# Optimization experiments

Measured on AMD Instinct MI355X. Metric: run time of the kernel, lower is better.

Reference implementation:

```python
import jax, jax.numpy as jnp
import numpy as np

D_MODEL = 1024
D_STATE = 16
D_CONV = 4
EXPAND = 2
D_INNER = D_MODEL * EXPAND


def setup_inputs() -> dict:
    key = jax.random.key(0)
    ks = jax.random.split(key, 10)
    B, L = 2, 2048
    x = jax.random.normal(ks[0], (B, L, D_MODEL), jnp.float32)
    W_in = jax.random.normal(ks[1], (2 * D_INNER, D_MODEL), jnp.float32) * (1.0 / np.sqrt(D_MODEL))
    conv_w = jax.random.normal(ks[2], (D_INNER, 1, D_CONV), jnp.float32) * (1.0 / np.sqrt(D_CONV))
    conv_b = jax.random.normal(ks[3], (D_INNER,), jnp.float32) * 0.1
    W_x = jax.random.normal(ks[4], (2 * D_STATE + 1, D_INNER), jnp.float32) * (1.0 / np.sqrt(D_INNER))
    A_log = jnp.log(jnp.abs(jax.random.normal(ks[5], (D_INNER, D_STATE), jnp.float32)) + 1e-4)
    D_param = jnp.ones((D_INNER,), jnp.float32)
    W_dt = jax.random.normal(ks[6], (D_INNER, 1), jnp.float32)
    b_dt = jax.random.normal(ks[7], (D_INNER,), jnp.float32) * 0.1
    W_out = jax.random.normal(ks[8], (D_MODEL, D_INNER), jnp.float32) * (1.0 / np.sqrt(D_INNER))
    return {"x": x, "W_in": W_in, "conv_w": conv_w, "conv_b": conv_b, "W_x": W_x,
            "A_log": A_log, "D_param": D_param, "W_dt": W_dt, "b_dt": b_dt, "W_out": W_out}


def _forward(x, W_in, conv_w, conv_b, W_x, A_log, D_param, W_dt, b_dt, W_out):
    B, L, _ = x.shape
    xz = x @ W_in.T                                  # [B,L,2*d_inner]
    x_ssm, z = jnp.split(xz, 2, axis=-1)
    # causal depthwise conv: torch pads both sides d_conv-1 then truncates to L == left-pad only
    xc = jnp.transpose(x_ssm, (0, 2, 1))             # [B,d_inner,L]
    xc = jax.lax.conv_general_dilated(
        xc, conv_w, window_strides=(1,), padding=[(D_CONV - 1, 0)],
        feature_group_count=D_INNER, dimension_numbers=("NCH", "OIH", "NCH"))
    xc = xc + conv_b[None, :, None]
    x_ssm = jax.nn.silu(jnp.transpose(xc, (0, 2, 1)))  # [B,L,d_inner]
    proj = x_ssm @ W_x.T                              # [B,L,2*d_state+1]
    B_ssm = proj[..., :D_STATE]                       # [B,L,d_state]
    C_ssm = proj[..., D_STATE:2 * D_STATE]            # [B,L,d_state]
    dt = jax.nn.softplus(proj[..., -1:] * W_dt[:, 0] + b_dt)  # [B,L,d_inner]
    A = -jnp.exp(A_log)                               # [d_inner,d_state]

    def step(h, inp):
        dt_t, Bt, Ct, xt = inp                        # [B,d_inner],[B,n],[B,n],[B,d_inner]
        dA = jnp.exp(dt_t[..., None] * A)             # [B,d_inner,d_state]
        h = dA * h + (xt * dt_t)[..., None] * Bt[:, None, :]
        y = jnp.einsum("bdn,bn->bd", h, Ct)
        return h, y

    h0 = jnp.zeros((B, D_INNER, D_STATE), x.dtype)
    inputs = (jnp.transpose(dt, (1, 0, 2)), jnp.transpose(B_ssm, (1, 0, 2)),
              jnp.transpose(C_ssm, (1, 0, 2)), jnp.transpose(x_ssm, (1, 0, 2)))
    _, ys = jax.lax.scan(step, h0, inputs)            # ys: [L,B,d_inner]
    y = jnp.transpose(ys, (1, 0, 2)) + x_ssm * D_param
    y = y * jax.nn.silu(z)
    return y @ W_out.T


def reference(x, W_in, conv_w, conv_b, W_x, A_log, D_param, W_dt, b_dt, W_out):
    return _forward(x, W_in, conv_w, conv_b, W_x, A_log, D_param, W_dt, b_dt, W_out)
```

## Files before the change

kernel.cpp:

```cpp
#include <hip/hip_runtime.h>
#include <hip/hip_bf16.h>
#include <cstddef>

#define DMODEL 1024
#define DI     2048
#define DS     16
#define LSEQ   2048
#define BATCH  2
#define NC     128
#define TCH    (LSEQ / NC)

typedef __attribute__((ext_vector_type(8))) short short8;
typedef __attribute__((ext_vector_type(4))) float f32x4;
typedef __attribute__((ext_vector_type(2))) float f32x2;
typedef __attribute__((ext_vector_type(8))) unsigned short us8;

__device__ __forceinline__ unsigned short f2bf(float f) {
    unsigned int u = __float_as_uint(f);
    unsigned int r = (u + 0x7fff + ((u >> 16) & 1)) >> 16;
    return (unsigned short)r;
}
__device__ __forceinline__ float bf2f(unsigned short b) {
    return __uint_as_float(((unsigned int)b) << 16);
}

__device__ __forceinline__ float fexp2(float x) {
#if __has_builtin(__builtin_amdgcn_exp2f)
    return __builtin_amdgcn_exp2f(x);
#else
    return exp2f(x);
#endif
}
__device__ __forceinline__ float flog2(float x) {
#if __has_builtin(__builtin_amdgcn_logf)
    return __builtin_amdgcn_logf(x);
#else
    return log2f(x);
#endif
}

#define LOG2E 1.4426950408889634f
#define RLOG2E 0.6931471805599453f

__device__ __forceinline__ float softplus_f(float v) {
    return (v > 20.f) ? v : flog2(1.f + fexp2(v * LOG2E)) * RLOG2E;
}

__device__ __forceinline__ void gload_lds16(const void* g, void* l) {
    __builtin_amdgcn_global_load_lds(
        (const __attribute__((address_space(1))) unsigned int*)g,
        (__attribute__((address_space(3))) unsigned int*)l, 16, 0, 0);
}

__device__ __forceinline__ void cvt8_store(const float* __restrict__ in,
                                           unsigned short* __restrict__ out, int i) {
    const float4* p = reinterpret_cast<const float4*>(in) + (size_t)i * 2;
    float4 v0 = p[0], v1 = p[1];
    us8 o;
    o[0] = f2bf(v0.x); o[1] = f2bf(v0.y); o[2] = f2bf(v0.z); o[3] = f2bf(v0.w);
    o[4] = f2bf(v1.x); o[5] = f2bf(v1.y); o[6] = f2bf(v1.z); o[7] = f2bf(v1.w);
    *reinterpret_cast<us8*>(out + (size_t)i * 8) = o;
}

#define PREP_X   524288
#define PREP_WI  (PREP_X + 524288)
#define PREP_WO  (PREP_WI + 262144)
#define PREP_WX  (PREP_WO + 12288)
#define PREP_A   (PREP_WX + 32768)
__global__ void prep_all(const float* __restrict__ x, const float* __restrict__ W_in,
                         const float* __restrict__ W_out, const float* __restrict__ wx,
                         const float* __restrict__ A_log,
                         unsigned short* __restrict__ Xb, unsigned short* __restrict__ W_inb,
                         unsigned short* __restrict__ W_outb, unsigned short* __restrict__ Wxb48,
                         float* __restrict__ At2) {
    int i = blockIdx.x * 256 + threadIdx.x;
    if (i < PREP_X) {
        cvt8_store(x, Xb, i);
    } else if (i < PREP_WI) {
        cvt8_store(W_in, W_inb, i - PREP_X);
    } else if (i < PREP_WO) {
        cvt8_store(W_out, W_outb, i - PREP_WI);
    } else if (i < PREP_WX) {
        int j = i - PREP_WO;
        size_t o = (size_t)j * 8;
        int row = (int)(o >> 11);
        if (row < 33) cvt8_store(wx, Wxb48, j);
        else *reinterpret_cast<us8*>(Wxb48 + o) = (us8)0;
    } else if (i < PREP_A) {
        int j = i - PREP_WX;
        int n = j / DI, d = j % DI;
        At2[j] = -__expf(A_log[d * DS + n]) * LOG2E;
    }
}

#define NTK1 32
__global__ __launch_bounds__(512, 4)
void gemm1_2b(const unsigned short* __restrict__ A, const unsigned short* __restrict__ B,
              unsigned short* __restrict__ C) {
    __shared__ unsigned short As[2][128 * 32];
    __shared__ unsigned short Bs[2][256 * 32];

    const int tid = threadIdx.x;
    const int wid = tid >> 6, ln = tid & 63;
    const int wm = wid >> 2, wn = wid & 3;

    int wg = blockIdx.x;
    wg = (wg & 7) * 64 + (wg >> 3);
    const int m0 = (wg >> 4) * 128;
    const int n0 = (wg & 15) * 256;

    const int srow = tid >> 2;
    const int sun  = tid & 3;
    const int ksrc = ((sun ^ ((srow >> 1) & 3)) * 8);

    const int fr = ln & 15;
    const int fku = (ln >> 4);

    f32x4 acc[4][4] = {};

    #define STAGE1(kt, c)                                                                  \
        do {                                                                               \
            gload_lds16(A + (size_t)(m0 + srow) * 1024 + (kt) * 32 + ksrc,                 \
                        &As[c][srow * 32 + sun * 8]);                                      \
            gload_lds16(B + (size_t)(n0 + srow) * 1024 + (kt) * 32 + ksrc,                 \
                        &Bs[c][srow * 32 + sun * 8]);                                      \
            gload_lds16(B + (size_t)(n0 + 128 + srow) * 1024 + (kt) * 32 + ksrc,           \
                        &Bs[c][(128 + srow) * 32 + sun * 8]);                              \
        } while (0)

    STAGE1(0, 0);
    asm volatile("s_waitcnt vmcnt(0)" ::: "memory");
    __builtin_amdgcn_s_barrier();
    __builtin_amdgcn_sched_barrier(0);

    for (int kt = 0; kt < NTK1; ++kt) {
        const int c = kt & 1;
        if (kt + 1 < NTK1) STAGE1(kt + 1, c ^ 1);

        short8 af[4], bfr[4];
        #pragma unroll
        for (int i = 0; i < 4; ++i) {
            int r = wm * 64 + i * 16 + fr;
            int u = fku ^ ((r >> 1) & 3);
            af[i] = *reinterpret_cast<const short8*>(&As[c][r * 32 + u * 8]);
        }
        #pragma unroll
        for (int j = 0; j < 4; ++j) {
            int r = wn * 64 + j * 16 + fr;
            int u = fku ^ ((r >> 1) & 3);
            bfr[j] = *reinterpret_cast<const short8*>(&Bs[c][r * 32 + u * 8]);
        }
        __builtin_amdgcn_sched_barrier(0);
        __builtin_amdgcn_s_setprio(1);
        #pragma unroll
        for (int i = 0; i < 4; ++i)
            #pragma unroll
            for (int j = 0; j < 4; ++j)
                acc[i][j] = __builtin_amdgcn_mfma_f32_16x16x32_bf16(af[i], bfr[j], acc[i][j], 0, 0, 0);
        __builtin_amdgcn_s_setprio(0);
        __builtin_amdgcn_sched_barrier(0);

        if (kt + 1 < NTK1) asm volatile("s_waitcnt vmcnt(0)" ::: "memory");
        __builtin_amdgcn_s_barrier();
        __builtin_amdgcn_sched_barrier(0);
    }
    #undef STAGE1

    const int cr = (ln >> 4) * 4, cc = ln & 15;
    #pragma unroll
    for (int i = 0; i < 4; ++i) {
        int row = m0 + wm * 64 + i * 16 + cr;
        #pragma unroll
        for (int j = 0; j < 4; ++j) {
            int col = n0 + wn * 64 + j * 16 + cc;
            #pragma unroll
            for (int r = 0; r < 4; ++r)
                C[(size_t)(row + r) * 4096 + col] = f2bf(acc[i][j][r]);
        }
    }
}

#define NT3 64
__global__ __launch_bounds__(256, 2)
void gemm3_pipe(const unsigned short* __restrict__ A,
                const unsigned short* __restrict__ B,
                float* __restrict__ C) {
    __shared__ unsigned short As[4][128 * 32];
    __shared__ unsigned short Bs[4][64 * 32];

    const int tid = threadIdx.x;
    const int wid = tid >> 6, ln = tid & 63;
    const int wm = wid >> 1, wn = wid & 1;

    int wg = blockIdx.x;
    wg = (wg & 7) * 64 + (wg >> 3);
    const int m0 = (wg >> 4) * 128;
    const int n0 = (wg & 15) * 64;

    const int srow = tid >> 2;
    const int sun  = tid & 3;
    const int ksrc = ((sun ^ ((srow >> 1) & 3)) * 8);

    const int fr = ln & 15;
    const int fku = (ln >> 4);

    f32x4 acc[4][2] = {};

    #define STAGE3(kt)                                                                     \
        do {                                                                               \
            const int bq_ = (kt) & 3;                                                      \
            gload_lds16(A + (size_t)(m0 + srow) * 2048 + (kt) * 32 + ksrc,                 \
                        &As[bq_][srow * 32 + sun * 8]);                                    \
            gload_lds16(A + (size_t)(m0 + 64 + srow) * 2048 + (kt) * 32 + ksrc,            \
                        &As[bq_][(64 + srow) * 32 + sun * 8]);                             \
            gload_lds16(B + (size_t)(n0 + srow) * 2048 + (kt) * 32 + ksrc,                 \
                        &Bs[bq_][srow * 32 + sun * 8]);                                    \
        } while (0)

    STAGE3(0); STAGE3(1); STAGE3(2);
    asm volatile("s_waitcnt vmcnt(6)" ::: "memory");
    __builtin_amdgcn_s_barrier();
    __builtin_amdgcn_sched_barrier(0);

    for (int kt = 0; kt < NT3; ++kt) {
        const int bq = kt & 3;
        if (kt + 3 < NT3) STAGE3(kt + 3);

        short8 af[4], bfr[2];
        #pragma unroll
        for (int i = 0; i < 4; ++i) {
            int r = wm * 64 + i * 16 + fr;
            int u = fku ^ ((r >> 1) & 3);
            af[i] = *reinterpret_cast<const short8*>(&As[bq][r * 32 + u * 8]);
        }
        #pragma unroll
        for (int j = 0; j < 2; ++j) {
            int r = wn * 32 + j * 16 + fr;
            int u = fku ^ ((r >> 1) & 3);
            bfr[j] = *reinterpret_cast<const short8*>(&Bs[bq][r * 32 + u * 8]);
        }
        __builtin_amdgcn_sched_barrier(0);
        __builtin_amdgcn_s_setprio(1);
        #pragma unroll
        for (int i = 0; i < 4; ++i)
            #pragma unroll
            for (int j = 0; j < 2; ++j)
                acc[i][j] = __builtin_amdgcn_mfma_f32_16x16x32_bf16(af[i], bfr[j], acc[i][j], 0, 0, 0);
        __builtin_amdgcn_s_setprio(0);
        __builtin_amdgcn_sched_barrier(0);

        if (kt < NT3 - 3)       asm volatile("s_waitcnt vmcnt(6)" ::: "memory");
        else if (kt == NT3 - 3) asm volatile("s_waitcnt vmcnt(3)" ::: "memory");
        else if (kt == NT3 - 2) asm volatile("s_waitcnt vmcnt(0)" ::: "memory");
        __builtin_amdgcn_s_barrier();
        __builtin_amdgcn_sched_barrier(0);
    }
    #undef STAGE3

    const int cr = (ln >> 4) * 4, cc = ln & 15;
    #pragma unroll
    for (int i = 0; i < 4; ++i) {
        int row = m0 + wm * 64 + i * 16 + cr;
        #pragma unroll
        for (int j = 0; j < 2; ++j) {
            int col = n0 + wn * 32 + j * 16 + cc;
            #pragma unroll
            for (int r = 0; r < 4; ++r)
                C[(size_t)(row + r) * 1024 + col] = acc[i][j][r];
        }
    }
}

#define RAWS 40
__global__ __launch_bounds__(256)
void gemm_proj_conv(const unsigned short* __restrict__ XZb, const unsigned short* __restrict__ Wxb,
                    const float* __restrict__ cw, const float* __restrict__ cb,
                    float* __restrict__ projp) {
    __shared__ unsigned short raw[67 * RAWS];
    __shared__ unsigned short Bs[48 * 32];

    const int tid = threadIdx.x;
    const int wv = tid >> 6, ln = tid & 63;
    const int m0 = blockIdx.x * 64;
    const int kz = blockIdx.y;
    const int srow = tid >> 2, skoff = (tid & 3) * 8;
    const int fr = ln & 15;
    const int lhat = wv * 16 + fr;
    const int d0 = (ln >> 4) * 8;

    const bool mstart = ((m0 & 2047) == 0);
    const int colbase = kz * 128;

    f32x4 acc[3] = {};

    for (int k0 = 0; k0 < 128; k0 += 32) {
        for (int j = tid; j < 268; j += 256) {
            int i = j >> 2, slot = j & 3;
            us8 v;
            if (mstart && i < 3) {
                v = (us8)0;
            } else {
                v = *reinterpret_cast<const us8*>(
                    XZb + (size_t)(m0 - 3 + i) * 4096 + colbase + k0 + slot * 8);
            }
            *reinterpret_cast<us8*>(&raw[i * RAWS + slot * 8]) = v;
        }
        if (wv < 3)
            gload_lds16(Wxb + (size_t)srow * 2048 + colbase + k0 + skoff, &Bs[wv * 512]);
        __syncthreads();

        short8 af;
        #pragma unroll
        for (int e = 0; e < 8; ++e) {
            int dg = colbase + k0 + d0 + e;
            float a = cb[dg];
            float4 w = *reinterpret_cast<const float4*>(cw + dg * 4);
            a += bf2f(raw[(lhat + 0) * RAWS + d0 + e]) * w.x;
            a += bf2f(raw[(lhat + 1) * RAWS + d0 + e]) * w.y;
            a += bf2f(raw[(lhat + 2) * RAWS + d0 + e]) * w.z;
            a += bf2f(raw[(lhat + 3) * RAWS + d0 + e]) * w.w;
            float v = a / (1.f + __expf(-a));
            ((unsigned short*)&af)[e] = (short)f2bf(v);
        }

        #pragma unroll
        for (int j = 0; j < 3; ++j) {
            short8 bf_ = *reinterpret_cast<const short8*>(&Bs[(j * 16 + fr) * 32 + d0]);
            acc[j] = __builtin_amdgcn_mfma_f32_16x16x32_bf16(af, bf_, acc[j], 0, 0, 0);
        }
        __syncthreads();
    }

    const int cr = (ln >> 4) * 4, cc = ln & 15;
    #pragma unroll
    for (int j = 0; j < 3; ++j) {
        int col = j * 16 + cc;
        if (col < 33) {
            #pragma unroll
            for (int r = 0; r < 4; ++r) {
                int row = m0 + wv * 16 + cr + r;
                projp[(size_t)row * 576 + kz * 36 + col] = acc[j][r];
            }
        }
    }
}

__global__ void proj_combine(const float* __restrict__ projp, float* __restrict__ proj) {
    int idx = blockIdx.x * 256 + threadIdx.x;
    if (idx >= BATCH * LSEQ * 33) return;
    int row = idx / 33, col = idx % 33;
    const float* pp = projp + (size_t)row * 576 + col;
    float s = 0.f;
    #pragma unroll
    for (int kz = 0; kz < 16; ++kz)
        s += pp[kz * 36];
    proj[(size_t)row * 36 + col] = s;
}

__global__ __launch_bounds__(256)
void scan_phase1(const unsigned short* __restrict__ XZb, const float* __restrict__ proj,
                 const float* __restrict__ At2, const float* __restrict__ W_dt,
                 const float* __restrict__ b_dt, const float* __restrict__ Dp,
                 const float* __restrict__ cw, const float* __restrict__ cb,
                 unsigned short* __restrict__ Hend,
                 float* __restrict__ dtsum, unsigned short* __restrict__ yloc) {
    const int d = blockIdx.x * 256 + threadIdx.x;
    const int c = blockIdx.y;
    const int b = blockIdx.z;
    const size_t r0 = (size_t)(b * LSEQ + c * TCH);

    f32x2 A2[DS / 2], h2[DS / 2];
    #pragma unroll
    for (int p = 0; p < DS / 2; ++p) {
        A2[p] = (f32x2){At2[(2 * p) * DI + d], At2[(2 * p + 1) * DI + d]};
        h2[p] = (f32x2){0.f, 0.f};
    }
    const float wdt = W_dt[d], bdt = b_dt[d], Dv = Dp[d];
    const float4 w = *reinterpret_cast<const float4*>(cw + d * 4);
    const float cbv = cb[d];

    float r3, r2, r1;
    if (c == 0) {
        r3 = r2 = r1 = 0.f;
    } else {
        r3 = bf2f(XZb[(r0 - 3) * 4096 + d]);
        r2 = bf2f(XZb[(r0 - 2) * 4096 + d]);
        r1 = bf2f(XZb[(r0 - 1) * 4096 + d]);
    }
    float ssum = 0.f;

    #pragma unroll 2
    for (int rl = 0; rl < TCH; ++rl) {
        const size_t row = r0 + rl;
        const float* pr = proj + row * 36;
        float dt = softplus_f(pr[32] * wdt + bdt);
        ssum += dt;
        float rr = bf2f(XZb[row * 4096 + d]);
        float a = cbv + r3 * w.x + r2 * w.y + r1 * w.z + rr * w.w;
        r3 = r2; r2 = r1; r1 = rr;
        float v = a / (1.f + __expf(-a));
        float x = bf2f(f2bf(v));
        float xdt = x * dt;
        f32x2 xdt2 = (f32x2){xdt, xdt};
        f32x2 y2 = (f32x2){0.f, 0.f};
        #pragma unroll
        for (int p = 0; p < DS / 2; ++p) {
            f32x2 t = A2[p] * dt;
            f32x2 e2 = (f32x2){fexp2(t.x), fexp2(t.y)};
            h2[p] = e2 * h2[p] + xdt2 * (f32x2){pr[2 * p], pr[2 * p + 1]};
            y2 += h2[p] * (f32x2){pr[16 + 2 * p], pr[17 + 2 * p]};
        }
        yloc[row * DI + d] = f2bf(y2.x + y2.y + x * Dv);
    }
    size_t base = ((size_t)(b * NC + c) * DS) * DI + d;
    #pragma unroll
    for (int p = 0; p < DS / 2; ++p) {
        Hend[base + (size_t)(2 * p) * DI]     = f2bf(h2[p].x);
        Hend[base + (size_t)(2 * p + 1) * DI] = f2bf(h2[p].y);
    }
    dtsum[(size_t)(b * NC + c) * DI + d] = ssum;
}

__global__ void scan_phase2(unsigned short* __restrict__ H, const float* __restrict__ dtsum,
                            const float* __restrict__ At2) {
    int idx = blockIdx.x * 256 + threadIdx.x;
    int b = idx / (DS * DI);
    int r = idx % (DS * DI);
    int n = r / DI, d = r % DI;
    float A2 = At2[n * DI + d];
    float h = 0.f;
    #pragma unroll 4
    for (int c = 0; c < NC; ++c) {
        size_t off = ((size_t)(b * NC + c) * DS + n) * DI + d;
        float He = bf2f(H[off]);
        float P = fexp2(A2 * dtsum[(size_t)(b * NC + c) * DI + d]);
        H[off] = f2bf(h);
        h = P * h + He;
    }
}

__global__ __launch_bounds__(256)
void scan_phase3(const unsigned short* __restrict__ yloc,
                 const float* __restrict__ proj, const float* __restrict__ At2,
                 const float* __restrict__ W_dt, const float* __restrict__ b_dt,
                 const unsigned short* __restrict__ Hin,
                 const unsigned short* __restrict__ XZb,
                 unsigned short* __restrict__ YB2) {
    const int tid = threadIdx.x;
    const int d = blockIdx.x * 256 + tid;
    const int c = blockIdx.y;
    const int b = blockIdx.z;
    const size_t r0 = (size_t)(b * LSEQ + c * TCH);

    f32x2 A2[DS / 2], Hn2[DS / 2];
    size_t hbase = ((size_t)(b * NC + c) * DS) * DI + d;
    #pragma unroll
    for (int p = 0; p < DS / 2; ++p) {
        A2[p]  = (f32x2){At2[(2 * p) * DI + d], At2[(2 * p + 1) * DI + d]};
        Hn2[p] = (f32x2){bf2f(Hin[hbase + (size_t)(2 * p) * DI]),
                         bf2f(Hin[hbase + (size_t)(2 * p + 1) * DI])};
    }
    const float wdt = W_dt[d], bdt = b_dt[d];
    float S = 0.f;

    #pragma unroll 2
    for (int rl = 0; rl < TCH; ++rl) {
        const size_t row = r0 + rl;
        const float* pr = proj + row * 36;
        float dt = softplus_f(pr[32] * wdt + bdt);
        S += dt;
        float yl = bf2f(yloc[row * DI + d]);
        float z  = bf2f(XZb[row * 4096 + 2048 + d]);
        f32x2 corr2 = (f32x2){0.f, 0.f};
        #pragma unroll
        for (int p = 0; p < DS / 2; ++p) {
            f32x2 t = A2[p] * S;
            f32x2 e2 = (f32x2){fexp2(t.x), fexp2(t.y)};
            corr2 += (f32x2){pr[16 + 2 * p], pr[17 + 2 * p]} * e2 * Hn2[p];
        }
        float y = yl + corr2.x + corr2.y;
        float sz = z / (1.f + __expf(-z));
        YB2[row * DI + d] = f2bf(y * sz);
    }
}

extern "C" void kernel_launch(void* const* d_in, const int* in_sizes, int n_in,
                              void* d_out, int out_size, void* d_ws, size_t ws_size,
                              hipStream_t stream) {
    const float* x      = (const float*)d_in[0];
    const float* W_in   = (const float*)d_in[1];
    const float* conv_w = (const float*)d_in[2];
    const float* conv_b = (const float*)d_in[3];
    const float* W_x    = (const float*)d_in[4];
    const float* A_log  = (const float*)d_in[5];
    const float* Dp     = (const float*)d_in[6];
    const float* W_dt   = (const float*)d_in[7];
    const float* b_dt   = (const float*)d_in[8];
    const float* W_out  = (const float*)d_in[9];
    float* out = (float*)d_out;

    char* ws = (char*)d_ws;
    unsigned short* XZb   = (unsigned short*)(ws + 0);
    float* PROJP = (float*)(ws + 33554432);
    unsigned short* Xb    = (unsigned short*)(ws + 50331648);
    unsigned short* W_inb = (unsigned short*)(ws + 58720256);
    unsigned short* YB2   = (unsigned short*)(ws + 50331648);
    unsigned short* Hbuf  = (unsigned short*)(ws + 67108864);
    unsigned short* YLOC  = (unsigned short*)(ws + 83886080);
    float* PROJ  = (float*)(ws + 100663296);
    float* DTSUM = (float*)(ws + 101711872);
    float* Abuf  = (float*)(ws + 106954752);
    unsigned short* W_outb = (unsigned short*)(ws + 108003328);
    unsigned short* Wxb48  = (unsigned short*)(ws + 112197632);

    const int M = BATCH * LSEQ;

    prep_all<<<(PREP_A + 255) / 256, 256, 0, stream>>>(
        x, W_in, W_out, W_x, A_log, Xb, W_inb, W_outb, Wxb48, Abuf);

    gemm1_2b<<<512, 512, 0, stream>>>(Xb, W_inb, XZb);

    gemm_proj_conv<<<dim3(M / 64, 16), 256, 0, stream>>>(
        XZb, Wxb48, conv_w, conv_b, PROJP);
    proj_combine<<<(M * 33 + 255) / 256, 256, 0, stream>>>(PROJP, PROJ);

    scan_phase1<<<dim3(DI / 256, NC, BATCH), 256, 0, stream>>>(
        XZb, PROJ, Abuf, W_dt, b_dt, Dp, conv_w, conv_b, Hbuf, DTSUM, YLOC);
    scan_phase2<<<BATCH * DS * DI / 256, 256, 0, stream>>>(Hbuf, DTSUM, Abuf);
    scan_phase3<<<dim3(DI / 256, NC, BATCH), 256, 0, stream>>>(
        YLOC, PROJ, Abuf, W_dt, b_dt, Hbuf, XZb, YB2);

    gemm3_pipe<<<512, 256, 0, stream>>>(YB2, W_outb, out);
}
```

Before: 182.7 us.

## Recompute chunk scan from carried state in phase 3 instead of storing local outputs

Phase 1 now only computes each chunk's end state and dt sum, with no per-row output. Phase 3 starts from the carried-in state, re-runs the full recurrence (conv, silu, exp and state update), and produces y directly. This removes the bf16 yloc write and read and the correction term that used the cumulative dt sum. In exchange, phase 3 recomputes the conv and the exponentials that phase 1 already did.

```diff
diff --git a/kernel.cpp b/kernel.cpp
--- a/kernel.cpp
+++ b/kernel.cpp
@@ -360,10 +360,9 @@
 __global__ __launch_bounds__(256)
 void scan_phase1(const unsigned short* __restrict__ XZb, const float* __restrict__ proj,
                  const float* __restrict__ At2, const float* __restrict__ W_dt,
-                 const float* __restrict__ b_dt, const float* __restrict__ Dp,
+                 const float* __restrict__ b_dt,
                  const float* __restrict__ cw, const float* __restrict__ cb,
-                 unsigned short* __restrict__ Hend,
-                 float* __restrict__ dtsum, unsigned short* __restrict__ yloc) {
+                 unsigned short* __restrict__ Hend, float* __restrict__ dtsum) {
     const int d = blockIdx.x * 256 + threadIdx.x;
     const int c = blockIdx.y;
     const int b = blockIdx.z;
@@ -375,7 +374,7 @@
         A2[p] = (f32x2){At2[(2 * p) * DI + d], At2[(2 * p + 1) * DI + d]};
         h2[p] = (f32x2){0.f, 0.f};
     }
-    const float wdt = W_dt[d], bdt = b_dt[d], Dv = Dp[d];
+    const float wdt = W_dt[d], bdt = b_dt[d];
     const float4 w = *reinterpret_cast<const float4*>(cw + d * 4);
     const float cbv = cb[d];
 
@@ -402,15 +401,12 @@
         float x = bf2f(f2bf(v));
         float xdt = x * dt;
         f32x2 xdt2 = (f32x2){xdt, xdt};
-        f32x2 y2 = (f32x2){0.f, 0.f};
         #pragma unroll
         for (int p = 0; p < DS / 2; ++p) {
             f32x2 t = A2[p] * dt;
             f32x2 e2 = (f32x2){fexp2(t.x), fexp2(t.y)};
             h2[p] = e2 * h2[p] + xdt2 * (f32x2){pr[2 * p], pr[2 * p + 1]};
-            y2 += h2[p] * (f32x2){pr[16 + 2 * p], pr[17 + 2 * p]};
-        }
-        yloc[row * DI + d] = f2bf(y2.x + y2.y + x * Dv);
+        }
     }
     size_t base = ((size_t)(b * NC + c) * DS) * DI + d;
     #pragma unroll
@@ -440,11 +436,11 @@
 }
 
 __global__ __launch_bounds__(256)
-void scan_phase3(const unsigned short* __restrict__ yloc,
-                 const float* __restrict__ proj, const float* __restrict__ At2,
-                 const float* __restrict__ W_dt, const float* __restrict__ b_dt,
+void scan_phase3(const unsigned short* __restrict__ XZb, const float* __restrict__ proj,
+                 const float* __restrict__ At2, const float* __restrict__ W_dt,
+                 const float* __restrict__ b_dt, const float* __restrict__ Dp,
+                 const float* __restrict__ cw, const float* __restrict__ cb,
                  const unsigned short* __restrict__ Hin,
-                 const unsigned short* __restrict__ XZb,
                  unsigned short* __restrict__ YB2) {
     const int tid = threadIdx.x;
     const int d = blockIdx.x * 256 + tid;
@@ -452,33 +448,49 @@
     const int b = blockIdx.z;
     const size_t r0 = (size_t)(b * LSEQ + c * TCH);
 
-    f32x2 A2[DS / 2], Hn2[DS / 2];
+    f32x2 A2[DS / 2], h2[DS / 2];
     size_t hbase = ((size_t)(b * NC + c) * DS) * DI + d;
     #pragma unroll
     for (int p = 0; p < DS / 2; ++p) {
-        A2[p]  = (f32x2){At2[(2 * p) * DI + d], At2[(2 * p + 1) * DI + d]};
-        Hn2[p] = (f32x2){bf2f(Hin[hbase + (size_t)(2 * p) * DI]),
-                         bf2f(Hin[hbase + (size_t)(2 * p + 1) * DI])};
-    }
-    const float wdt = W_dt[d], bdt = b_dt[d];
-    float S = 0.f;
+        A2[p] = (f32x2){At2[(2 * p) * DI + d], At2[(2 * p + 1) * DI + d]};
+        h2[p] = (f32x2){bf2f(Hin[hbase + (size_t)(2 * p) * DI]),
+                        bf2f(Hin[hbase + (size_t)(2 * p + 1) * DI])};
+    }
+    const float wdt = W_dt[d], bdt = b_dt[d], Dv = Dp[d];
+    const float4 w = *reinterpret_cast<const float4*>(cw + d * 4);
+    const float cbv = cb[d];
+
+    float r3, r2, r1;
+    if (c == 0) {
+        r3 = r2 = r1 = 0.f;
+    } else {
+        r3 = bf2f(XZb[(r0 - 3) * 4096 + d]);
+        r2 = bf2f(XZb[(r0 - 2) * 4096 + d]);
+        r1 = bf2f(XZb[(r0 - 1) * 4096 + d]);
+    }
 
     #pragma unroll 2
     for (int rl = 0; rl < TCH; ++rl) {
         const size_t row = r0 + rl;
         const float* pr = proj + row * 36;
         float dt = softplus_f(pr[32] * wdt + bdt);
-        S += dt;
-        float yl = bf2f(yloc[row * DI + d]);
-        float z  = bf2f(XZb[row * 4096 + 2048 + d]);
-        f32x2 corr2 = (f32x2){0.f, 0.f};
+        float rr = bf2f(XZb[row * 4096 + d]);
+        float a = cbv + r3 * w.x + r2 * w.y + r1 * w.z + rr * w.w;
+        r3 = r2; r2 = r1; r1 = rr;
+        float v = a / (1.f + __expf(-a));
+        float x = bf2f(f2bf(v));
+        float xdt = x * dt;
+        f32x2 xdt2 = (f32x2){xdt, xdt};
+        f32x2 y2 = (f32x2){0.f, 0.f};
         #pragma unroll
         for (int p = 0; p < DS / 2; ++p) {
-            f32x2 t = A2[p] * S;
+            f32x2 t = A2[p] * dt;
             f32x2 e2 = (f32x2){fexp2(t.x), fexp2(t.y)};
-            corr2 += (f32x2){pr[16 + 2 * p], pr[17 + 2 * p]} * e2 * Hn2[p];
-        }
-        float y = yl + corr2.x + corr2.y;
+            h2[p] = e2 * h2[p] + xdt2 * (f32x2){pr[2 * p], pr[2 * p + 1]};
+            y2 += h2[p] * (f32x2){pr[16 + 2 * p], pr[17 + 2 * p]};
+        }
+        float y = y2.x + y2.y + x * Dv;
+        float z = bf2f(XZb[row * 4096 + 2048 + d]);
         float sz = z / (1.f + __expf(-z));
         YB2[row * DI + d] = f2bf(y * sz);
     }
@@ -506,7 +518,6 @@
     unsigned short* W_inb = (unsigned short*)(ws + 58720256);
     unsigned short* YB2   = (unsigned short*)(ws + 50331648);
     unsigned short* Hbuf  = (unsigned short*)(ws + 67108864);
-    unsigned short* YLOC  = (unsigned short*)(ws + 83886080);
     float* PROJ  = (float*)(ws + 100663296);
     float* DTSUM = (float*)(ws + 101711872);
     float* Abuf  = (float*)(ws + 106954752);
@@ -525,10 +536,10 @@
     proj_combine<<<(M * 33 + 255) / 256, 256, 0, stream>>>(PROJP, PROJ);
 
     scan_phase1<<<dim3(DI / 256, NC, BATCH), 256, 0, stream>>>(
-        XZb, PROJ, Abuf, W_dt, b_dt, Dp, conv_w, conv_b, Hbuf, DTSUM, YLOC);
+        XZb, PROJ, Abuf, W_dt, b_dt, conv_w, conv_b, Hbuf, DTSUM);
     scan_phase2<<<BATCH * DS * DI / 256, 256, 0, stream>>>(Hbuf, DTSUM, Abuf);
     scan_phase3<<<dim3(DI / 256, NC, BATCH), 256, 0, stream>>>(
-        YLOC, PROJ, Abuf, W_dt, b_dt, Hbuf, XZb, YB2);
+        XZb, PROJ, Abuf, W_dt, b_dt, Dp, conv_w, conv_b, Hbuf, YB2);
 
     gemm3_pipe<<<512, 256, 0, stream>>>(YB2, W_outb, out);
 }
```

New measurement: 186.4 us. +2.0%, slower.

## Parallelize chunk-carry scan with wavefront shuffle prefix scan over chunks

Applied to the files above, without the earlier changes.

Phase 2 of the chunked selective scan previously ran a serial loop over 128 chunks per (batch, state, channel) thread. It now assigns one 64-lane wavefront per (batch, state, channel), with each lane holding two chunks, and computes the carried states with a Hillis-Steele associative scan over (decay, state) pairs using shuffles. This removes the long serial dependency chain, but memory access becomes strided across chunks, so each wave touches scattered addresses rather than coalesced channel-contiguous ones, and the launch grid grows 64x.

```diff
diff --git a/kernel.cpp b/kernel.cpp
--- a/kernel.cpp
+++ b/kernel.cpp
@@ -421,22 +421,43 @@
     dtsum[(size_t)(b * NC + c) * DI + d] = ssum;
 }
 
-__global__ void scan_phase2(unsigned short* __restrict__ H, const float* __restrict__ dtsum,
-                            const float* __restrict__ At2) {
-    int idx = blockIdx.x * 256 + threadIdx.x;
-    int b = idx / (DS * DI);
-    int r = idx % (DS * DI);
-    int n = r / DI, d = r % DI;
-    float A2 = At2[n * DI + d];
-    float h = 0.f;
-    #pragma unroll 4
-    for (int c = 0; c < NC; ++c) {
-        size_t off = ((size_t)(b * NC + c) * DS + n) * DI + d;
-        float He = bf2f(H[off]);
-        float P = fexp2(A2 * dtsum[(size_t)(b * NC + c) * DI + d]);
-        H[off] = f2bf(h);
-        h = P * h + He;
-    }
+__global__ __launch_bounds__(256)
+void scan_phase2(unsigned short* __restrict__ H, const float* __restrict__ dtsum,
+                 const float* __restrict__ At2) {
+    const int tid = threadIdx.x;
+    const int ln = tid & 63;
+    const int widx = blockIdx.x * 4 + (tid >> 6);
+    const int b = widx / (DS * DI);
+    const int r = widx % (DS * DI);
+    const int n = r / DI, d = r % DI;
+    const float A2 = At2[n * DI + d];
+
+    const size_t off0 = ((size_t)(b * NC + ln) * DS + n) * DI + d;
+    const size_t off1 = ((size_t)(b * NC + 64 + ln) * DS + n) * DI + d;
+    float He0 = bf2f(H[off0]);
+    float He1 = bf2f(H[off1]);
+    float P0 = fexp2(A2 * dtsum[(size_t)(b * NC + ln) * DI + d]);
+    float P1 = fexp2(A2 * dtsum[(size_t)(b * NC + 64 + ln) * DI + d]);
+
+    #pragma unroll
+    for (int s = 1; s < 64; s <<= 1) {
+        float Pp0 = __shfl_up(P0, s), Hp0 = __shfl_up(He0, s);
+        float Pp1 = __shfl_up(P1, s), Hp1 = __shfl_up(He1, s);
+        if (ln >= s) {
+            He0 = P0 * Hp0 + He0;  P0 = P0 * Pp0;
+            He1 = P1 * Hp1 + He1;  P1 = P1 * Pp1;
+        }
+    }
+    float Ht0 = __shfl(He0, 63);
+
+    float hin0 = __shfl_up(He0, 1);
+    if (ln == 0) hin0 = 0.f;
+    float Pex1 = __shfl_up(P1, 1), Hex1 = __shfl_up(He1, 1);
+    if (ln == 0) { Pex1 = 1.f; Hex1 = 0.f; }
+    float hin1 = Pex1 * Ht0 + Hex1;
+
+    H[off0] = f2bf(hin0);
+    H[off1] = f2bf(hin1);
 }
 
 __global__ __launch_bounds__(256)
@@ -526,7 +547,7 @@
 
     scan_phase1<<<dim3(DI / 256, NC, BATCH), 256, 0, stream>>>(
         XZb, PROJ, Abuf, W_dt, b_dt, Dp, conv_w, conv_b, Hbuf, DTSUM, YLOC);
-    scan_phase2<<<BATCH * DS * DI / 256, 256, 0, stream>>>(Hbuf, DTSUM, Abuf);
+    scan_phase2<<<BATCH * DS * DI / 4, 256, 0, stream>>>(Hbuf, DTSUM, Abuf);
     scan_phase3<<<dim3(DI / 256, NC, BATCH), 256, 0, stream>>>(
         YLOC, PROJ, Abuf, W_dt, b_dt, Hbuf, XZb, YB2);
 
```

New measurement: 247.3 us. +35.4%, slower.
